# Optimization experiments

Hardware: AMD Instinct MI355X
Metric: run time of the kernel (lower is better)

## Reference

```python
import jax, jax.numpy as jnp
import numpy as np
import math

NUM_HEADS = 16


def rotate_half(x):
    # faithful to torch: take even/odd interleaved halves, cat(-x2, x1)
    x1 = x[..., ::2]
    x2 = x[..., 1::2]
    return jnp.concatenate((-x2, x1), axis=-1)


def rotary_tables(seq_len, head_dim, dtype):
    inv_freq = 1.0 / (10000.0 ** (jnp.arange(0, head_dim, 2, dtype=jnp.float32) / head_dim))
    t = jnp.arange(seq_len, dtype=jnp.float32)
    freqs = t[:, None] * inv_freq[None, :]           # [T, hd/2]
    emb = jnp.concatenate((freqs, freqs), axis=-1)   # [T, hd]
    cos = jnp.cos(emb)[None, None, :, :].astype(dtype)
    sin = jnp.sin(emb)[None, None, :, :].astype(dtype)
    return cos, sin


def setup_inputs() -> dict:
    key = jax.random.key(0)
    k1, k2, k3, k4 = jax.random.split(key, 4)
    B, T, D = 2, 2048, 1024
    scale = 1.0 / math.sqrt(D)
    x = jax.random.normal(k1, (B, T, D), dtype=jnp.float32)
    w_qkv = jax.random.normal(k2, (3 * D, D), dtype=jnp.float32) * scale
    w_out = jax.random.normal(k3, (D, D), dtype=jnp.float32) * scale
    b_out = jax.random.normal(k4, (D,), dtype=jnp.float32) * scale
    return {"x": x, "w_qkv": w_qkv, "w_out": w_out, "b_out": b_out}


def reference(x, w_qkv, w_out, b_out):
    B, T, D = x.shape
    H = NUM_HEADS
    hd = D // H

    qkv = x @ w_qkv.T                                # [B, T, 3D]
    q, k, v = jnp.split(qkv, 3, axis=-1)
    def to_heads(a):
        return a.reshape(B, T, H, hd).transpose(0, 2, 1, 3)  # [B, H, T, hd]
    q, k, v = to_heads(q), to_heads(k), to_heads(v)

    cos, sin = rotary_tables(T, hd, x.dtype)
    q = q * cos + rotate_half(q) * sin
    k = k * cos + rotate_half(k) * sin

    attn = jnp.einsum("bhqd,bhkd->bhqk", q, k) / math.sqrt(hd)
    attn = jax.nn.softmax(attn, axis=-1)
    out = jnp.einsum("bhqk,bhkd->bhqd", attn, v)
    out = out.transpose(0, 2, 1, 3).reshape(B, T, D)
    return out @ w_out.T + b_out
```

## Files before the change

### kernel.cpp

```cpp
#include <hip/hip_runtime.h>
#include <math.h>

#define B_ 2
#define T_ 2048
#define D_ 1024
#define H_ 16

typedef __attribute__((ext_vector_type(8))) short bf16x8;
typedef __attribute__((ext_vector_type(4))) float f32x4;
typedef __attribute__((address_space(3))) char lds_char;
typedef __attribute__((address_space(1))) const char g_char;

static __device__ inline unsigned short bf16_rne(float f) {
    union { float f; unsigned u; } v; v.f = f;
    unsigned r = v.u + 0x7FFFu + ((v.u >> 16) & 1u);
    return (unsigned short)(r >> 16);
}
static __device__ inline unsigned pack2bf(float lo, float hi) {
    return (unsigned)bf16_rne(lo) | ((unsigned)bf16_rne(hi) << 16);
}

__global__ __launch_bounds__(256) void split_kernel(const float* __restrict__ in,
                                                    unsigned short* __restrict__ hi,
                                                    unsigned short* __restrict__ lo,
                                                    int n8) {
    int i = blockIdx.x * 256 + threadIdx.x;
    if (i >= n8) return;
    const float4* ip = (const float4*)in + (size_t)i * 2;
    float4 f0 = ip[0], f1 = ip[1];
    float fs[8] = {f0.x, f0.y, f0.z, f0.w, f1.x, f1.y, f1.z, f1.w};
    unsigned hu[4], lu[4];
#pragma unroll
    for (int j = 0; j < 4; ++j) {
        unsigned short h0 = bf16_rne(fs[2 * j]), h1 = bf16_rne(fs[2 * j + 1]);
        union { unsigned u; float f; } c0, c1;
        c0.u = (unsigned)h0 << 16; c1.u = (unsigned)h1 << 16;
        unsigned short l0 = bf16_rne(fs[2 * j] - c0.f);
        unsigned short l1 = bf16_rne(fs[2 * j + 1] - c1.f);
        hu[j] = (unsigned)h0 | ((unsigned)h1 << 16);
        lu[j] = (unsigned)l0 | ((unsigned)l1 << 16);
    }
    *(uint4*)(hi + (size_t)i * 8) = make_uint4(hu[0], hu[1], hu[2], hu[3]);
    *(uint4*)(lo + (size_t)i * 8) = make_uint4(lu[0], lu[1], lu[2], lu[3]);
}

__global__ __launch_bounds__(256) void rope_tables(float* __restrict__ cosT,
                                                   float* __restrict__ sinT) {
    int idx = blockIdx.x * 256 + threadIdx.x;
    int t = idx >> 5, i = idx & 31;
    double invf_d = exp(-((double)(2 * i) / 64.0) * 9.210340371976184);
    float invf = (float)invf_d;
    float ang = (float)t * invf;
    cosT[idx] = (float)cos((double)ang);
    sinT[idx] = (float)sin((double)ang);
}

__global__ __launch_bounds__(256) void rope_apply(float* __restrict__ qkv,
                                                  const float* __restrict__ cosT,
                                                  const float* __restrict__ sinT) {
    int idx = blockIdx.x * 256 + threadIdx.x;
    int h = idx & 15;
    int sel = (idx >> 4) & 1;
    int t = (idx >> 5) & 2047;
    int b = idx >> 16;
    float* p = qkv + ((size_t)(b * T_ + t)) * 3072 + sel * 1024 + h * 64;
    float v[64];
#pragma unroll
    for (int d = 0; d < 64; d += 4) {
        float4 f = *reinterpret_cast<const float4*>(p + d);
        v[d] = f.x; v[d + 1] = f.y; v[d + 2] = f.z; v[d + 3] = f.w;
    }
    const float* c = cosT + t * 32;
    const float* s = sinT + t * 32;
    float o[64];
#pragma unroll
    for (int i = 0; i < 32; ++i) {
        float ci = c[i], si = s[i];
        o[i]      = v[i]      * ci - v[2 * i + 1] * si;
        o[i + 32] = v[i + 32] * ci + v[2 * i]     * si;
    }
#pragma unroll
    for (int d = 0; d < 64; d += 4) {
        float4 f;
        f.x = o[d]; f.y = o[d + 1]; f.z = o[d + 2]; f.w = o[d + 3];
        *reinterpret_cast<float4*>(p + d) = f;
    }
}

template <int BIAS>
__global__ __launch_bounds__(256) void gemm_split(const unsigned short* __restrict__ Ahi,
                                                  const unsigned short* __restrict__ Alo,
                                                  const unsigned short* __restrict__ Bhi,
                                                  const unsigned short* __restrict__ Blo,
                                                  const float* __restrict__ bias,
                                                  float* __restrict__ C,
                                                  int M, int N, int K) {
    __shared__ alignas(16) char lds[32768];
    char* As_hi = lds;
    char* As_lo = lds + 8192;
    char* Bs_hi = lds + 16384;
    char* Bs_lo = lds + 24576;

    const int tid = threadIdx.x, l = tid & 63, w = tid >> 6;
    const int m0 = blockIdx.y * 128, n0 = blockIdx.x * 128;
    const int wr = (w >> 1) * 64, wc = (w & 1) * 64;
    const int q16 = l & 15, g8 = l >> 4;
    const int srow = w * 16 + (l >> 2);

    f32x4 acc[4][4];
#pragma unroll
    for (int i = 0; i < 4; ++i)
#pragma unroll
        for (int j = 0; j < 4; ++j) acc[i][j] = (f32x4){0.f, 0.f, 0.f, 0.f};

    for (int k0 = 0; k0 < K; k0 += 32) {
#pragma unroll
        for (int rd = 0; rd < 2; ++rd) {
            int row = srow + rd * 64;
            int g = (l & 3) ^ (row & 3);
            size_t goffA = (size_t)(m0 + row) * K + k0 + g * 8;
            size_t goffB = (size_t)(n0 + row) * K + k0 + g * 8;
            int lbase = rd * 4096 + w * 1024;
            __builtin_amdgcn_global_load_lds((g_char*)(Ahi + goffA), (lds_char*)(As_hi + lbase), 16, 0, 0);
            __builtin_amdgcn_global_load_lds((g_char*)(Alo + goffA), (lds_char*)(As_lo + lbase), 16, 0, 0);
            __builtin_amdgcn_global_load_lds((g_char*)(Bhi + goffB), (lds_char*)(Bs_hi + lbase), 16, 0, 0);
            __builtin_amdgcn_global_load_lds((g_char*)(Blo + goffB), (lds_char*)(Bs_lo + lbase), 16, 0, 0);
        }
        __syncthreads();

        bf16x8 ah[4], al[4], bh[4], bl[4];
#pragma unroll
        for (int i = 0; i < 4; ++i) {
            int ra = wr + 16 * i + q16, rb = wc + 16 * i + q16;
            ah[i] = *(const bf16x8*)(As_hi + ra * 64 + ((g8 ^ (ra & 3)) * 16));
            al[i] = *(const bf16x8*)(As_lo + ra * 64 + ((g8 ^ (ra & 3)) * 16));
            bh[i] = *(const bf16x8*)(Bs_hi + rb * 64 + ((g8 ^ (rb & 3)) * 16));
            bl[i] = *(const bf16x8*)(Bs_lo + rb * 64 + ((g8 ^ (rb & 3)) * 16));
        }
#pragma unroll
        for (int i = 0; i < 4; ++i)
#pragma unroll
            for (int j = 0; j < 4; ++j) {
                acc[i][j] = __builtin_amdgcn_mfma_f32_16x16x32_bf16(ah[i], bh[j], acc[i][j], 0, 0, 0);
                acc[i][j] = __builtin_amdgcn_mfma_f32_16x16x32_bf16(ah[i], bl[j], acc[i][j], 0, 0, 0);
                acc[i][j] = __builtin_amdgcn_mfma_f32_16x16x32_bf16(al[i], bh[j], acc[i][j], 0, 0, 0);
            }
        __syncthreads();
    }

#pragma unroll
    for (int i = 0; i < 4; ++i)
#pragma unroll
        for (int j = 0; j < 4; ++j) {
            int col = n0 + wc + 16 * j + q16;
            float badd = BIAS ? bias[col] : 0.f;
#pragma unroll
            for (int r = 0; r < 4; ++r) {
                int row = m0 + wr + 16 * i + 4 * g8 + r;
                C[(size_t)row * N + col] = acc[i][j][r] + badd;
            }
        }
}

static __device__ inline void stage_rowmajor(char* lds, const float* g,
                                             float scale, int tid) {
#pragma unroll
    for (int i = 0; i < 4; ++i) {
        int idx = tid + 256 * i;
        int row = idx >> 4, c = idx & 15;
        float4 f = *reinterpret_cast<const float4*>(g + (size_t)row * 3072 + c * 4);
        unsigned lo = pack2bf(f.x * scale, f.y * scale);
        unsigned hi = pack2bf(f.z * scale, f.w * scale);
        int byte = row * 128 + ((c * 8) ^ ((row & 7) << 4));
        *reinterpret_cast<unsigned long long*>(lds + byte) =
            (unsigned long long)lo | ((unsigned long long)hi << 32);
    }
}

static __device__ inline void stage_v_t(char* lds, const float* g, int tid) {
    int c = tid & 15, r = tid >> 4;
    int n0 = c * 4, kv0 = r * 4;
    float4 f0 = *reinterpret_cast<const float4*>(g + (size_t)(kv0 + 0) * 3072 + n0);
    float4 f1 = *reinterpret_cast<const float4*>(g + (size_t)(kv0 + 1) * 3072 + n0);
    float4 f2 = *reinterpret_cast<const float4*>(g + (size_t)(kv0 + 2) * 3072 + n0);
    float4 f3 = *reinterpret_cast<const float4*>(g + (size_t)(kv0 + 3) * 3072 + n0);
    const float* a0 = &f0.x; const float* a1 = &f1.x;
    const float* a2 = &f2.x; const float* a3 = &f3.x;
#pragma unroll
    for (int j = 0; j < 4; ++j) {
        int n = n0 + j;
        unsigned lo = pack2bf(a0[j], a1[j]);
        unsigned hi = pack2bf(a2[j], a3[j]);
        int byte = n * 128 + ((kv0 * 2) ^ ((n & 7) << 4));
        *reinterpret_cast<unsigned long long*>(lds + byte) =
            (unsigned long long)lo | ((unsigned long long)hi << 32);
    }
}

static __device__ inline bf16x8 frag_read(const char* lds, int row, int elem0) {
    int byte = row * 128 + ((elem0 * 2) ^ ((row & 7) << 4));
    return *reinterpret_cast<const bf16x8*>(lds + byte);
}

__global__ __launch_bounds__(256) void attn_mfma(const float* __restrict__ qkv,
                                                 float* __restrict__ ctx) {
    __shared__ unsigned long long ldsbuf[3072];
    char* q_lds  = (char*)ldsbuf;
    char* k_lds  = q_lds + 8192;
    char* vt_lds = q_lds + 16384;

    const int tid  = threadIdx.x;
    const int w    = tid >> 6;
    const int lane = tid & 63;
    const int g    = lane >> 4;
    const int q    = lane & 15;

    const int qb = blockIdx.x;
    const int bh = blockIdx.y;
    const int b  = bh >> 4, h = bh & 15;

    const float* base = qkv + (size_t)b * T_ * 3072;
    const float* Qg = base + (size_t)(qb * 64) * 3072 + h * 64;
    const float* Kg = base + 1024 + h * 64;
    const float* Vg = base + 2048 + h * 64;

    stage_rowmajor(q_lds, Qg, 0.125f, tid);
    stage_rowmajor(k_lds, Kg, 1.0f, tid);
    stage_v_t(vt_lds, Vg, tid);
    __syncthreads();

    const int qrow = 16 * w + q;
    bf16x8 bq0 = frag_read(q_lds, qrow, 8 * g);
    bf16x8 bq1 = frag_read(q_lds, qrow, 32 + 8 * g);

    f32x4 acc[4];
#pragma unroll
    for (int i = 0; i < 4; ++i) acc[i] = (f32x4){0.f, 0.f, 0.f, 0.f};
    float mrun = -INFINITY, lrun = 0.f;

    const int srcA = q + 32 * (g & 1);
    const int srcB = srcA + 16;
    const bool hiSel = (g >> 1) != 0;

    for (int kt = 0; kt < 32; ++kt) {
        f32x4 st[4];
#pragma unroll
        for (int mt = 0; mt < 4; ++mt) {
            int kvrow = 16 * mt + q;
            f32x4 c = (f32x4){0.f, 0.f, 0.f, 0.f};
            c = __builtin_amdgcn_mfma_f32_16x16x32_bf16(
                    frag_read(k_lds, kvrow, 8 * g), bq0, c, 0, 0, 0);
            c = __builtin_amdgcn_mfma_f32_16x16x32_bf16(
                    frag_read(k_lds, kvrow, 32 + 8 * g), bq1, c, 0, 0, 0);
            st[mt] = c;
        }

        float tmax = -INFINITY;
#pragma unroll
        for (int mt = 0; mt < 4; ++mt)
#pragma unroll
            for (int r = 0; r < 4; ++r) tmax = fmaxf(tmax, st[mt][r]);
        tmax = fmaxf(tmax, __shfl_xor(tmax, 16));
        tmax = fmaxf(tmax, __shfl_xor(tmax, 32));
        float mnew = fmaxf(mrun, tmax);
        float corr = __expf(mrun - mnew);
        mrun = mnew;

        float p[16];
        float tsum = 0.f;
#pragma unroll
        for (int mt = 0; mt < 4; ++mt)
#pragma unroll
            for (int r = 0; r < 4; ++r) {
                float e = __expf(st[mt][r] - mnew);
                p[4 * mt + r] = e;
                tsum += e;
            }
        tsum += __shfl_xor(tsum, 16);
        tsum += __shfl_xor(tsum, 32);
        lrun = lrun * corr + tsum;
#pragma unroll
        for (int i = 0; i < 4; ++i) {
            acc[i][0] *= corr; acc[i][1] *= corr;
            acc[i][2] *= corr; acc[i][3] *= corr;
        }

        unsigned pk0[4], pk1[4];
#pragma unroll
        for (int mt = 0; mt < 4; ++mt) {
            pk0[mt] = pack2bf(p[4 * mt + 0], p[4 * mt + 1]);
            pk1[mt] = pack2bf(p[4 * mt + 2], p[4 * mt + 3]);
        }
        union { bf16x8 v; unsigned u[4]; } bp0, bp1;
        {
            unsigned xa0 = __shfl(pk0[0], srcA), ya0 = __shfl(pk0[1], srcA);
            unsigned xa1 = __shfl(pk1[0], srcA), ya1 = __shfl(pk1[1], srcA);
            unsigned xb0 = __shfl(pk0[0], srcB), yb0 = __shfl(pk0[1], srcB);
            unsigned xb1 = __shfl(pk1[0], srcB), yb1 = __shfl(pk1[1], srcB);
            bp0.u[0] = hiSel ? ya0 : xa0;
            bp0.u[1] = hiSel ? ya1 : xa1;
            bp0.u[2] = hiSel ? yb0 : xb0;
            bp0.u[3] = hiSel ? yb1 : xb1;
        }
        {
            unsigned xa0 = __shfl(pk0[2], srcA), ya0 = __shfl(pk0[3], srcA);
            unsigned xa1 = __shfl(pk1[2], srcA), ya1 = __shfl(pk1[3], srcA);
            unsigned xb0 = __shfl(pk0[2], srcB), yb0 = __shfl(pk0[3], srcB);
            unsigned xb1 = __shfl(pk1[2], srcB), yb1 = __shfl(pk1[3], srcB);
            bp1.u[0] = hiSel ? ya0 : xa0;
            bp1.u[1] = hiSel ? ya1 : xa1;
            bp1.u[2] = hiSel ? yb0 : xb0;
            bp1.u[3] = hiSel ? yb1 : xb1;
        }

#pragma unroll
        for (int nt = 0; nt < 4; ++nt) {
            int nrow = 16 * nt + q;
            acc[nt] = __builtin_amdgcn_mfma_f32_16x16x32_bf16(
                          frag_read(vt_lds, nrow, 8 * g), bp0.v, acc[nt], 0, 0, 0);
            acc[nt] = __builtin_amdgcn_mfma_f32_16x16x32_bf16(
                          frag_read(vt_lds, nrow, 32 + 8 * g), bp1.v, acc[nt], 0, 0, 0);
        }

        __syncthreads();
        if (kt < 31) {
            stage_rowmajor(k_lds, Kg + (size_t)(kt + 1) * 64 * 3072, 1.0f, tid);
            stage_v_t(vt_lds, Vg + (size_t)(kt + 1) * 64 * 3072, tid);
            __syncthreads();
        }
    }

    float inv_l = 1.0f / lrun;
    const int q_abs = qb * 64 + 16 * w + q;
    float* outp = ctx + ((size_t)b * T_ + q_abs) * 1024 + h * 64;
#pragma unroll
    for (int nt = 0; nt < 4; ++nt)
#pragma unroll
        for (int r = 0; r < 4; ++r)
            outp[16 * nt + 4 * g + r] = acc[nt][r] * inv_l;
}

extern "C" void kernel_launch(void* const* d_in, const int* in_sizes, int n_in,
                              void* d_out, int out_size, void* d_ws, size_t ws_size,
                              hipStream_t stream) {
    const float* x     = (const float*)d_in[0];
    const float* w_qkv = (const float*)d_in[1];
    const float* w_out = (const float*)d_in[2];
    const float* b_out = (const float*)d_in[3];
    float* out = (float*)d_out;

    char* base = (char*)d_ws;
    float* qkvF = (float*)base;
    unsigned short* ctx_hi  = (unsigned short*)(base + 0);
    unsigned short* ctx_lo  = (unsigned short*)(base + 8388608);
    unsigned short* wout_hi = (unsigned short*)(base + 16777216);
    unsigned short* wout_lo = (unsigned short*)(base + 18874368);
    unsigned short* x_hi = (unsigned short*)(base + 50331648);
    unsigned short* x_lo = (unsigned short*)(base + 58720256);
    float* ctxF = (float*)(base + 50331648);
    unsigned short* wq_hi = (unsigned short*)(base + 67108864);
    unsigned short* wq_lo = (unsigned short*)(base + 73400320);
    float* cosT = (float*)(base + 79691776);
    float* sinT = cosT + 65536;

    rope_tables<<<256, 256, 0, stream>>>(cosT, sinT);
    split_kernel<<<2048, 256, 0, stream>>>(x, x_hi, x_lo, 524288);
    split_kernel<<<1536, 256, 0, stream>>>(w_qkv, wq_hi, wq_lo, 393216);
    gemm_split<0><<<dim3(24, 32), 256, 0, stream>>>(x_hi, x_lo, wq_hi, wq_lo,
                                                    nullptr, qkvF, 4096, 3072, 1024);
    rope_apply<<<512, 256, 0, stream>>>(qkvF, cosT, sinT);
    attn_mfma<<<dim3(32, 32), 256, 0, stream>>>(qkvF, ctxF);
    split_kernel<<<2048, 256, 0, stream>>>(ctxF, ctx_hi, ctx_lo, 524288);
    split_kernel<<<512, 256, 0, stream>>>(w_out, wout_hi, wout_lo, 131072);
    gemm_split<1><<<dim3(8, 32), 256, 0, stream>>>(ctx_hi, ctx_lo, wout_hi, wout_lo,
                                                   b_out, out, 4096, 1024, 1024);
}
```

Before: 350.0 us.

## Pre-pack rotated Q/K and transposed V to bf16 and pipeline attention loads

Rope is fused into a new prep kernel that writes bf16 Q (prescaled by log2e/sqrt(hd)), bf16 K and a transposed bf16 V per head. The attention kernel double-buffers K/V tiles through async global-to-LDS loads and switches to exp2. It skips the rescale of the running max unless the new max exceeds a threshold. It raises wave priority around the MFMA blocks and writes the hi/lo split of the context directly, which removes the separate split pass. These changes cut fp32 re-reads and the per-tile conversion work, at the cost of a new kernel and an intermediate buffer, and the deferred rescale relies on the fp32 accumulators having enough headroom.

```diff
diff --git a/kernel.cpp b/kernel.cpp
--- a/kernel.cpp
+++ b/kernel.cpp
@@ -10,6 +10,9 @@
 typedef __attribute__((ext_vector_type(4))) float f32x4;
 typedef __attribute__((address_space(3))) char lds_char;
 typedef __attribute__((address_space(1))) const char g_char;
+
+#define QSCALE 0.18033688011112042f
+#define DEFER_THR 11.5f
 
 static __device__ inline unsigned short bf16_rne(float f) {
     union { float f; unsigned u; } v; v.f = f;
@@ -53,38 +56,6 @@
     float ang = (float)t * invf;
     cosT[idx] = (float)cos((double)ang);
     sinT[idx] = (float)sin((double)ang);
-}
-
-__global__ __launch_bounds__(256) void rope_apply(float* __restrict__ qkv,
-                                                  const float* __restrict__ cosT,
-                                                  const float* __restrict__ sinT) {
-    int idx = blockIdx.x * 256 + threadIdx.x;
-    int h = idx & 15;
-    int sel = (idx >> 4) & 1;
-    int t = (idx >> 5) & 2047;
-    int b = idx >> 16;
-    float* p = qkv + ((size_t)(b * T_ + t)) * 3072 + sel * 1024 + h * 64;
-    float v[64];
-#pragma unroll
-    for (int d = 0; d < 64; d += 4) {
-        float4 f = *reinterpret_cast<const float4*>(p + d);
-        v[d] = f.x; v[d + 1] = f.y; v[d + 2] = f.z; v[d + 3] = f.w;
-    }
-    const float* c = cosT + t * 32;
-    const float* s = sinT + t * 32;
-    float o[64];
-#pragma unroll
-    for (int i = 0; i < 32; ++i) {
-        float ci = c[i], si = s[i];
-        o[i]      = v[i]      * ci - v[2 * i + 1] * si;
-        o[i + 32] = v[i + 32] * ci + v[2 * i]     * si;
-    }
-#pragma unroll
-    for (int d = 0; d < 64; d += 4) {
-        float4 f;
-        f.x = o[d]; f.y = o[d + 1]; f.z = o[d + 2]; f.w = o[d + 3];
-        *reinterpret_cast<float4*>(p + d) = f;
-    }
 }
 
 template <int BIAS>
@@ -162,38 +133,74 @@
         }
 }
 
-static __device__ inline void stage_rowmajor(char* lds, const float* g,
-                                             float scale, int tid) {
-#pragma unroll
-    for (int i = 0; i < 4; ++i) {
-        int idx = tid + 256 * i;
-        int row = idx >> 4, c = idx & 15;
-        float4 f = *reinterpret_cast<const float4*>(g + (size_t)row * 3072 + c * 4);
-        unsigned lo = pack2bf(f.x * scale, f.y * scale);
-        unsigned hi = pack2bf(f.z * scale, f.w * scale);
-        int byte = row * 128 + ((c * 8) ^ ((row & 7) << 4));
-        *reinterpret_cast<unsigned long long*>(lds + byte) =
-            (unsigned long long)lo | ((unsigned long long)hi << 32);
-    }
-}
-
-static __device__ inline void stage_v_t(char* lds, const float* g, int tid) {
-    int c = tid & 15, r = tid >> 4;
-    int n0 = c * 4, kv0 = r * 4;
-    float4 f0 = *reinterpret_cast<const float4*>(g + (size_t)(kv0 + 0) * 3072 + n0);
-    float4 f1 = *reinterpret_cast<const float4*>(g + (size_t)(kv0 + 1) * 3072 + n0);
-    float4 f2 = *reinterpret_cast<const float4*>(g + (size_t)(kv0 + 2) * 3072 + n0);
-    float4 f3 = *reinterpret_cast<const float4*>(g + (size_t)(kv0 + 3) * 3072 + n0);
-    const float* a0 = &f0.x; const float* a1 = &f1.x;
-    const float* a2 = &f2.x; const float* a3 = &f3.x;
-#pragma unroll
-    for (int j = 0; j < 4; ++j) {
-        int n = n0 + j;
-        unsigned lo = pack2bf(a0[j], a1[j]);
-        unsigned hi = pack2bf(a2[j], a3[j]);
-        int byte = n * 128 + ((kv0 * 2) ^ ((n & 7) << 4));
-        *reinterpret_cast<unsigned long long*>(lds + byte) =
-            (unsigned long long)lo | ((unsigned long long)hi << 32);
+__global__ __launch_bounds__(256) void prep_attn(const float* __restrict__ qkv,
+                                                 const float* __restrict__ cosT,
+                                                 const float* __restrict__ sinT,
+                                                 unsigned short* __restrict__ qb,
+                                                 unsigned short* __restrict__ kb,
+                                                 unsigned short* __restrict__ vt) {
+    __shared__ float vlds[64][65];
+    const int tid = threadIdx.x;
+    const int t0 = blockIdx.x * 64;
+    const int bh = blockIdx.y;
+    const int b = bh >> 4, h = bh & 15;
+
+    if (tid < 128) {
+        int sel = tid >> 6;
+        int t = t0 + (tid & 63);
+        const float* p = qkv + ((size_t)(b * T_ + t)) * 3072 + sel * 1024 + h * 64;
+        float v[64];
+#pragma unroll
+        for (int d = 0; d < 64; d += 4) {
+            float4 f = *reinterpret_cast<const float4*>(p + d);
+            v[d] = f.x; v[d + 1] = f.y; v[d + 2] = f.z; v[d + 3] = f.w;
+        }
+        const float* c = cosT + t * 32;
+        const float* s = sinT + t * 32;
+        float o[64];
+#pragma unroll
+        for (int i = 0; i < 32; ++i) {
+            float ci = c[i], si = s[i];
+            o[i]      = v[i]      * ci - v[2 * i + 1] * si;
+            o[i + 32] = v[i + 32] * ci + v[2 * i]     * si;
+        }
+        float sc = sel ? 1.0f : QSCALE;
+        unsigned short* dst = (sel ? kb : qb) + ((size_t)bh * T_ + t) * 64;
+#pragma unroll
+        for (int d2 = 0; d2 < 8; ++d2) {
+            uint4 u;
+            u.x = pack2bf(o[8 * d2 + 0] * sc, o[8 * d2 + 1] * sc);
+            u.y = pack2bf(o[8 * d2 + 2] * sc, o[8 * d2 + 3] * sc);
+            u.z = pack2bf(o[8 * d2 + 4] * sc, o[8 * d2 + 5] * sc);
+            u.w = pack2bf(o[8 * d2 + 6] * sc, o[8 * d2 + 7] * sc);
+            *reinterpret_cast<uint4*>(dst + d2 * 8) = u;
+        }
+    } else {
+        int tt = tid - 128;
+        int row = tt >> 1, half = tt & 1;
+        const float* p = qkv + ((size_t)(b * T_ + t0 + row)) * 3072 + 2048 + h * 64 + half * 32;
+#pragma unroll
+        for (int j = 0; j < 8; ++j) {
+            float4 f = *reinterpret_cast<const float4*>(p + j * 4);
+            vlds[row][half * 32 + j * 4 + 0] = f.x;
+            vlds[row][half * 32 + j * 4 + 1] = f.y;
+            vlds[row][half * 32 + j * 4 + 2] = f.z;
+            vlds[row][half * 32 + j * 4 + 3] = f.w;
+        }
+    }
+    __syncthreads();
+    if (tid >= 128) {
+        int tt = tid - 128;
+        int d = tt >> 1, half = tt & 1;
+        unsigned out[16];
+#pragma unroll
+        for (int j = 0; j < 16; ++j)
+            out[j] = pack2bf(vlds[half * 32 + 2 * j][d], vlds[half * 32 + 2 * j + 1][d]);
+        unsigned short* dst = vt + ((size_t)bh * 64 + d) * T_ + t0 + half * 32;
+#pragma unroll
+        for (int j = 0; j < 4; ++j)
+            *reinterpret_cast<uint4*>(dst + j * 8) =
+                make_uint4(out[4 * j], out[4 * j + 1], out[4 * j + 2], out[4 * j + 3]);
     }
 }
 
@@ -202,12 +209,36 @@
     return *reinterpret_cast<const bf16x8*>(lds + byte);
 }
 
-__global__ __launch_bounds__(256) void attn_mfma(const float* __restrict__ qkv,
-                                                 float* __restrict__ ctx) {
-    __shared__ unsigned long long ldsbuf[3072];
-    char* q_lds  = (char*)ldsbuf;
-    char* k_lds  = q_lds + 8192;
-    char* vt_lds = q_lds + 16384;
+static __device__ inline void stage_contig(const unsigned short* gtile, char* ldst,
+                                           int w, int lane) {
+#pragma unroll
+    for (int n = 0; n < 2; ++n) {
+        int loff = n * 4096 + w * 1024;
+        int row = (loff >> 7) + (lane >> 3);
+        int g = (lane & 7) ^ (row & 7);
+        const unsigned short* src = gtile + row * 64 + g * 8;
+        __builtin_amdgcn_global_load_lds((g_char*)src, (lds_char*)(ldst + loff), 16, 0, 0);
+    }
+}
+
+static __device__ inline void stage_vt_tile(const unsigned short* vhead, int kt,
+                                            char* ldst, int w, int lane) {
+#pragma unroll
+    for (int n = 0; n < 2; ++n) {
+        int loff = n * 4096 + w * 1024;
+        int row = (loff >> 7) + (lane >> 3);
+        int g = (lane & 7) ^ (row & 7);
+        const unsigned short* src = vhead + (size_t)row * T_ + kt * 64 + g * 8;
+        __builtin_amdgcn_global_load_lds((g_char*)src, (lds_char*)(ldst + loff), 16, 0, 0);
+    }
+}
+
+__global__ __launch_bounds__(256) void attn_mfma(const unsigned short* __restrict__ qb,
+                                                 const unsigned short* __restrict__ kb,
+                                                 const unsigned short* __restrict__ vt,
+                                                 unsigned short* __restrict__ ctx_hi,
+                                                 unsigned short* __restrict__ ctx_lo) {
+    __shared__ alignas(16) char lds[40960];
 
     const int tid  = threadIdx.x;
     const int w    = tid >> 6;
@@ -215,23 +246,22 @@
     const int g    = lane >> 4;
     const int q    = lane & 15;
 
-    const int qb = blockIdx.x;
-    const int bh = blockIdx.y;
-    const int b  = bh >> 4, h = bh & 15;
-
-    const float* base = qkv + (size_t)b * T_ * 3072;
-    const float* Qg = base + (size_t)(qb * 64) * 3072 + h * 64;
-    const float* Kg = base + 1024 + h * 64;
-    const float* Vg = base + 2048 + h * 64;
-
-    stage_rowmajor(q_lds, Qg, 0.125f, tid);
-    stage_rowmajor(k_lds, Kg, 1.0f, tid);
-    stage_v_t(vt_lds, Vg, tid);
+    const int qbk = blockIdx.x;
+    const int bh  = blockIdx.y;
+    const int b   = bh >> 4, h = bh & 15;
+
+    const unsigned short* qtile = qb + ((size_t)bh * T_ + qbk * 64) * 64;
+    const unsigned short* khead = kb + (size_t)bh * T_ * 64;
+    const unsigned short* vhead = vt + (size_t)bh * 64 * T_;
+
+    stage_contig(qtile, lds, w, lane);
+    stage_contig(khead, lds + 8192, w, lane);
+    stage_vt_tile(vhead, 0, lds + 24576, w, lane);
     __syncthreads();
 
     const int qrow = 16 * w + q;
-    bf16x8 bq0 = frag_read(q_lds, qrow, 8 * g);
-    bf16x8 bq1 = frag_read(q_lds, qrow, 32 + 8 * g);
+    bf16x8 bq0 = frag_read(lds, qrow, 8 * g);
+    bf16x8 bq1 = frag_read(lds, qrow, 32 + 8 * g);
 
     f32x4 acc[4];
 #pragma unroll
@@ -243,47 +273,57 @@
     const bool hiSel = (g >> 1) != 0;
 
     for (int kt = 0; kt < 32; ++kt) {
+        const int cur = kt & 1;
+        if (kt < 31) {
+            stage_contig(khead + (size_t)(kt + 1) * 64 * 64, lds + 8192 + (cur ^ 1) * 8192, w, lane);
+            stage_vt_tile(vhead, kt + 1, lds + 24576 + (cur ^ 1) * 8192, w, lane);
+        }
+        const char* kc = lds + 8192 + cur * 8192;
+        const char* vc = lds + 24576 + cur * 8192;
+
         f32x4 st[4];
+        __builtin_amdgcn_s_setprio(1);
 #pragma unroll
         for (int mt = 0; mt < 4; ++mt) {
             int kvrow = 16 * mt + q;
             f32x4 c = (f32x4){0.f, 0.f, 0.f, 0.f};
-            c = __builtin_amdgcn_mfma_f32_16x16x32_bf16(
-                    frag_read(k_lds, kvrow, 8 * g), bq0, c, 0, 0, 0);
-            c = __builtin_amdgcn_mfma_f32_16x16x32_bf16(
-                    frag_read(k_lds, kvrow, 32 + 8 * g), bq1, c, 0, 0, 0);
+            c = __builtin_amdgcn_mfma_f32_16x16x32_bf16(frag_read(kc, kvrow, 8 * g), bq0, c, 0, 0, 0);
+            c = __builtin_amdgcn_mfma_f32_16x16x32_bf16(frag_read(kc, kvrow, 32 + 8 * g), bq1, c, 0, 0, 0);
             st[mt] = c;
         }
-
-        float tmax = -INFINITY;
+        __builtin_amdgcn_s_setprio(0);
+
+        float tmax = st[0][0];
 #pragma unroll
         for (int mt = 0; mt < 4; ++mt)
 #pragma unroll
             for (int r = 0; r < 4; ++r) tmax = fmaxf(tmax, st[mt][r]);
         tmax = fmaxf(tmax, __shfl_xor(tmax, 16));
         tmax = fmaxf(tmax, __shfl_xor(tmax, 32));
-        float mnew = fmaxf(mrun, tmax);
-        float corr = __expf(mrun - mnew);
-        mrun = mnew;
-
+        if (!__all(tmax - mrun <= DEFER_THR)) {
+            float mnew = fmaxf(mrun, tmax);
+            float corr = exp2f(mrun - mnew);
+            lrun *= corr;
+#pragma unroll
+            for (int i = 0; i < 4; ++i) {
+                acc[i][0] *= corr; acc[i][1] *= corr;
+                acc[i][2] *= corr; acc[i][3] *= corr;
+            }
+            mrun = mnew;
+        }
         float p[16];
         float tsum = 0.f;
 #pragma unroll
         for (int mt = 0; mt < 4; ++mt)
 #pragma unroll
             for (int r = 0; r < 4; ++r) {
-                float e = __expf(st[mt][r] - mnew);
+                float e = exp2f(st[mt][r] - mrun);
                 p[4 * mt + r] = e;
                 tsum += e;
             }
         tsum += __shfl_xor(tsum, 16);
         tsum += __shfl_xor(tsum, 32);
-        lrun = lrun * corr + tsum;
-#pragma unroll
-        for (int i = 0; i < 4; ++i) {
-            acc[i][0] *= corr; acc[i][1] *= corr;
-            acc[i][2] *= corr; acc[i][3] *= corr;
-        }
+        lrun += tsum;
 
         unsigned pk0[4], pk1[4];
 #pragma unroll
@@ -313,31 +353,32 @@
             bp1.u[3] = hiSel ? yb1 : xb1;
         }
 
+        __builtin_amdgcn_s_setprio(1);
 #pragma unroll
         for (int nt = 0; nt < 4; ++nt) {
             int nrow = 16 * nt + q;
-            acc[nt] = __builtin_amdgcn_mfma_f32_16x16x32_bf16(
-                          frag_read(vt_lds, nrow, 8 * g), bp0.v, acc[nt], 0, 0, 0);
-            acc[nt] = __builtin_amdgcn_mfma_f32_16x16x32_bf16(
-                          frag_read(vt_lds, nrow, 32 + 8 * g), bp1.v, acc[nt], 0, 0, 0);
-        }
+            acc[nt] = __builtin_amdgcn_mfma_f32_16x16x32_bf16(frag_read(vc, nrow, 8 * g), bp0.v, acc[nt], 0, 0, 0);
+            acc[nt] = __builtin_amdgcn_mfma_f32_16x16x32_bf16(frag_read(vc, nrow, 32 + 8 * g), bp1.v, acc[nt], 0, 0, 0);
+        }
+        __builtin_amdgcn_s_setprio(0);
 
         __syncthreads();
-        if (kt < 31) {
-            stage_rowmajor(k_lds, Kg + (size_t)(kt + 1) * 64 * 3072, 1.0f, tid);
-            stage_v_t(vt_lds, Vg + (size_t)(kt + 1) * 64 * 3072, tid);
-            __syncthreads();
-        }
     }
 
     float inv_l = 1.0f / lrun;
-    const int q_abs = qb * 64 + 16 * w + q;
-    float* outp = ctx + ((size_t)b * T_ + q_abs) * 1024 + h * 64;
+    const int q_abs = qbk * 64 + 16 * w + q;
+    size_t obase = ((size_t)b * T_ + q_abs) * 1024 + h * 64;
 #pragma unroll
     for (int nt = 0; nt < 4; ++nt)
 #pragma unroll
-        for (int r = 0; r < 4; ++r)
-            outp[16 * nt + 4 * g + r] = acc[nt][r] * inv_l;
+        for (int r = 0; r < 4; ++r) {
+            float o = acc[nt][r] * inv_l;
+            unsigned short hh = bf16_rne(o);
+            union { unsigned u; float f; } hf; hf.u = (unsigned)hh << 16;
+            unsigned short ll = bf16_rne(o - hf.f);
+            ctx_hi[obase + 16 * nt + 4 * g + r] = hh;
+            ctx_lo[obase + 16 * nt + 4 * g + r] = ll;
+        }
 }
 
 extern "C" void kernel_launch(void* const* d_in, const int* in_sizes, int n_in,
@@ -351,15 +392,17 @@
 
     char* base = (char*)d_ws;
     float* qkvF = (float*)base;
+    unsigned short* x_hi = (unsigned short*)(base + 50331648);
+    unsigned short* x_lo = (unsigned short*)(base + 58720256);
+    unsigned short* wq_hi = (unsigned short*)(base + 67108864);
+    unsigned short* wq_lo = (unsigned short*)(base + 73400320);
+    unsigned short* qb16 = (unsigned short*)(base + 50331648);
+    unsigned short* kb16 = (unsigned short*)(base + 58720256);
+    unsigned short* vt16 = (unsigned short*)(base + 67108864);
     unsigned short* ctx_hi  = (unsigned short*)(base + 0);
     unsigned short* ctx_lo  = (unsigned short*)(base + 8388608);
     unsigned short* wout_hi = (unsigned short*)(base + 16777216);
     unsigned short* wout_lo = (unsigned short*)(base + 18874368);
-    unsigned short* x_hi = (unsigned short*)(base + 50331648);
-    unsigned short* x_lo = (unsigned short*)(base + 58720256);
-    float* ctxF = (float*)(base + 50331648);
-    unsigned short* wq_hi = (unsigned short*)(base + 67108864);
-    unsigned short* wq_lo = (unsigned short*)(base + 73400320);
     float* cosT = (float*)(base + 79691776);
     float* sinT = cosT + 65536;
 
@@ -368,10 +411,9 @@
     split_kernel<<<1536, 256, 0, stream>>>(w_qkv, wq_hi, wq_lo, 393216);
     gemm_split<0><<<dim3(24, 32), 256, 0, stream>>>(x_hi, x_lo, wq_hi, wq_lo,
                                                     nullptr, qkvF, 4096, 3072, 1024);
-    rope_apply<<<512, 256, 0, stream>>>(qkvF, cosT, sinT);
-    attn_mfma<<<dim3(32, 32), 256, 0, stream>>>(qkvF, ctxF);
-    split_kernel<<<2048, 256, 0, stream>>>(ctxF, ctx_hi, ctx_lo, 524288);
+    prep_attn<<<dim3(32, 32), 256, 0, stream>>>(qkvF, cosT, sinT, qb16, kb16, vt16);
     split_kernel<<<512, 256, 0, stream>>>(w_out, wout_hi, wout_lo, 131072);
+    attn_mfma<<<dim3(32, 32), 256, 0, stream>>>(qb16, kb16, vt16, ctx_hi, ctx_lo);
     gemm_split<1><<<dim3(8, 32), 256, 0, stream>>>(ctx_hi, ctx_lo, wout_hi, wout_lo,
                                                    b_out, out, 4096, 1024, 1024);
 }
```

After: 324.8 us. -7.2%, faster.
